# Optimization experiments

Hardware: AMD Instinct MI355X
Metric: run time of the kernel (lower is better)

The kernel has to match this reference:

```python
import jax, jax.numpy as jnp
import numpy as np

SWIGLU_LIMIT = 7.0
ALPHA = 1.702

def swiglu(x):
    # interleaved gate/linear halves, clamped, as in the torch module
    x_glu = x[..., ::2]
    x_lin = x[..., 1::2]
    x_glu = jnp.minimum(x_glu, SWIGLU_LIMIT)
    x_lin = jnp.clip(x_lin, -SWIGLU_LIMIT, SWIGLU_LIMIT)
    return x_glu * jax.nn.sigmoid(ALPHA * x_glu) * (x_lin + 1.0)

def setup_inputs() -> dict:
    key = jax.random.key(0)
    ks = jax.random.split(key, 6)
    B, K, E, H, I = 1024, 4, 16, 2048, 2048
    t = jax.random.normal(ks[0], (B, H), dtype=jnp.float32)
    expert_indices = jax.random.randint(ks[1], (B, K), 0, E, dtype=jnp.int32)
    gate_up_proj = jax.random.normal(ks[2], (E, 2 * I, H), dtype=jnp.float32) * 0.02
    gate_up_proj_bias = jax.random.normal(ks[3], (E, 2 * I), dtype=jnp.float32) * 0.02
    down_proj = jax.random.normal(ks[4], (E, H, I), dtype=jnp.float32) * 0.02
    down_proj_bias = jax.random.normal(ks[5], (E, H), dtype=jnp.float32) * 0.02
    return {"t": t, "expert_indices": expert_indices,
            "gate_up_proj": gate_up_proj, "gate_up_proj_bias": gate_up_proj_bias,
            "down_proj": down_proj, "down_proj_bias": down_proj_bias}

def reference(t, expert_indices, gate_up_proj, gate_up_proj_bias, down_proj, down_proj_bias):
    # Math-equivalent to the torch per-token weight gather: compute every token
    # against every expert, then gather the top_k selected expert outputs.
    # This avoids materializing the [B, K, 2I, H] gathered weight tensor.
    h = jnp.einsum('eck,bk->bec', gate_up_proj, t) + gate_up_proj_bias[None]  # [B,E,2I]
    h = swiglu(h)                                                              # [B,E,I]
    o = jnp.einsum('eck,bek->bec', down_proj, h) + down_proj_bias[None]        # [B,E,H]
    out = jnp.take_along_axis(o, expert_indices[:, :, None].astype(jnp.int32), axis=1)  # [B,K,H]
    return out
```

## Files before the change

### kernel.cpp

```cpp
#include <hip/hip_runtime.h>

typedef unsigned int uint32;
typedef __attribute__((ext_vector_type(8))) short short8;
typedef __attribute__((ext_vector_type(4))) float floatx4;

#define B_TOK 1024
#define TOPK 4
#define NEXP 16
#define H_DIM 2048
#define I_DIM 2048
#define NSLOT 4096
#define CAP 512
#define C1 4096
#define SLOT_ROWS 8192

#define TM 128
#define TN 128
#define BK 32
#define NTH 256

__device__ __forceinline__ unsigned short f2bf(float x) {
  unsigned int u = __float_as_uint(x);
  u += 0x7fffu + ((u >> 16) & 1u);
  return (unsigned short)(u >> 16);
}

__device__ __forceinline__ uint32 pk2bf(float a, float b) {
  uint32 ua = __float_as_uint(a) + 0x8000u;
  uint32 ub = __float_as_uint(b) + 0x8000u;
  return __builtin_amdgcn_perm(ub, ua, 0x07060302u);
}

__global__ void k_setup(const float* __restrict__ t, unsigned short* __restrict__ t_bf,
                        int* __restrict__ sorted_slots, int* __restrict__ counts) {
  int gid = blockIdx.x * blockDim.x + threadIdx.x;
  const float4* tp = (const float4*)t;
  float4 v = tp[gid];
  ushort4 o;
  o.x = f2bf(v.x); o.y = f2bf(v.y); o.z = f2bf(v.z); o.w = f2bf(v.w);
  ((ushort4*)t_bf)[gid] = o;
  if (gid < SLOT_ROWS) sorted_slots[gid] = 0;
  if (gid < NEXP) counts[gid] = 0;
}

__global__ void k_scatter(const int* __restrict__ eidx,
                          int* __restrict__ sorted_slots, int* __restrict__ counts) {
  int slot = blockIdx.x * blockDim.x + threadIdx.x;
  if (slot >= NSLOT) return;
  int e = eidx[slot];
  int j = atomicAdd(counts + e, 1);
  if (j < CAP) sorted_slots[e * CAP + j] = slot;
}

__global__ __launch_bounds__(NTH) void k_gemm1(
    const unsigned short* __restrict__ t_bf, const float* __restrict__ Wg,
    const float* __restrict__ bg, const int* __restrict__ sorted_slots,
    const int* __restrict__ counts, unsigned short* __restrict__ h_act) {
  const int e = blockIdx.y >> 2;
  const int m0 = (blockIdx.y & 3) * TM;
  int cnt = counts[e]; cnt = cnt > CAP ? CAP : cnt;
  if (m0 >= cnt) return;
  const int mr = min(cnt - m0, TM);
  const int c0 = blockIdx.x * TN;
  const int base = e * CAP + m0;

  __shared__ unsigned short smA[2][TM * BK];
  __shared__ unsigned short smB[2][TN * BK];

  const int tid = threadIdx.x;
  const int kq = tid & 3;
  const int r0 = tid >> 2;
  const int r1 = r0 + 64;
  const int sw = (r0 >> 1) & 3;

  const int tok0 = sorted_slots[base + r0] >> 2;
  const int tok1 = sorted_slots[base + r1] >> 2;
  const unsigned short* pA0 = t_bf + (size_t)tok0 * H_DIM + kq * 8;
  const unsigned short* pA1 = t_bf + (size_t)tok1 * H_DIM + kq * 8;
  const float* pB0 = Wg + ((size_t)e * C1 + (size_t)(c0 + r0)) * H_DIM + kq * 8;
  const float* pB1 = Wg + ((size_t)e * C1 + (size_t)(c0 + r1)) * H_DIM + kq * 8;

  const int offA0 = r0 * BK + (kq ^ sw) * 8;
  const int offA1 = r1 * BK + (kq ^ sw) * 8;
  const int offB0 = offA0;
  const int offB1 = offA1;

  const int wave = tid >> 6;
  const int lane = tid & 63;
  const int wm = wave & 1, wn = wave >> 1;
  const int l15 = lane & 15;
  const int kc = lane >> 4;
  const int kcs = (kc ^ ((l15 >> 1) & 3)) * 8;

  floatx4 acc[4][4];
#pragma unroll
  for (int i = 0; i < 4; ++i)
#pragma unroll
    for (int j = 0; j < 4; ++j) acc[i][j] = (floatx4){0.f, 0.f, 0.f, 0.f};

  uint4 a0 = *(const uint4*)(pA0);
  uint4 a1 = *(const uint4*)(pA1);
  float4 b00 = *(const float4*)(pB0);
  float4 b01 = *(const float4*)(pB0 + 4);
  float4 b10 = *(const float4*)(pB1);
  float4 b11 = *(const float4*)(pB1 + 4);
  {
    *(uint4*)&smA[0][offA0] = a0;
    *(uint4*)&smA[0][offA1] = a1;
    uint4 w0, w1;
    w0.x = pk2bf(b00.x, b00.y); w0.y = pk2bf(b00.z, b00.w);
    w0.z = pk2bf(b01.x, b01.y); w0.w = pk2bf(b01.z, b01.w);
    w1.x = pk2bf(b10.x, b10.y); w1.y = pk2bf(b10.z, b10.w);
    w1.z = pk2bf(b11.x, b11.y); w1.w = pk2bf(b11.z, b11.w);
    *(uint4*)&smB[0][offB0] = w0;
    *(uint4*)&smB[0][offB1] = w1;
  }

  const int nk = H_DIM / BK;
#pragma unroll 2
  for (int kk = 0; kk < nk; ++kk) {
    __syncthreads();
    const int buf = kk & 1;
    const bool more = (kk + 1) < nk;
    if (more) {
      const int ko = (kk + 1) * BK;
      a0 = *(const uint4*)(pA0 + ko);
      a1 = *(const uint4*)(pA1 + ko);
      b00 = *(const float4*)(pB0 + ko);
      b01 = *(const float4*)(pB0 + ko + 4);
      b10 = *(const float4*)(pB1 + ko);
      b11 = *(const float4*)(pB1 + ko + 4);
    }
    short8 af[4], bfr[4];
#pragma unroll
    for (int i = 0; i < 4; ++i)
      af[i] = *(const short8*)&smA[buf][(wm * 64 + i * 16 + l15) * BK + kcs];
#pragma unroll
    for (int j = 0; j < 4; ++j)
      bfr[j] = *(const short8*)&smB[buf][(wn * 64 + j * 16 + l15) * BK + kcs];
#pragma unroll
    for (int i = 0; i < 4; ++i)
#pragma unroll
      for (int j = 0; j < 4; ++j)
        acc[i][j] = __builtin_amdgcn_mfma_f32_16x16x32_bf16(af[i], bfr[j], acc[i][j], 0, 0, 0);
    if (more) {
      *(uint4*)&smA[buf ^ 1][offA0] = a0;
      *(uint4*)&smA[buf ^ 1][offA1] = a1;
      uint4 w0, w1;
      w0.x = pk2bf(b00.x, b00.y); w0.y = pk2bf(b00.z, b00.w);
      w0.z = pk2bf(b01.x, b01.y); w0.w = pk2bf(b01.z, b01.w);
      w1.x = pk2bf(b10.x, b10.y); w1.y = pk2bf(b10.z, b10.w);
      w1.z = pk2bf(b11.x, b11.y); w1.w = pk2bf(b11.z, b11.w);
      *(uint4*)&smB[buf ^ 1][offB0] = w0;
      *(uint4*)&smB[buf ^ 1][offB1] = w1;
    }
  }

  const int rq = (lane >> 4) * 4;
#pragma unroll
  for (int j = 0; j < 4; ++j) {
    const int c = c0 + wn * 64 + j * 16 + l15;
    const float bias = bg[e * C1 + c];
    const int ic = c >> 1;
#pragma unroll
    for (int i = 0; i < 4; ++i) {
      const int rbase = wm * 64 + i * 16 + rq;
#pragma unroll
      for (int r = 0; r < 4; ++r) {
        float v = acc[i][j][r] + bias;
        float o = __shfl_xor(v, 1);
        if ((lane & 1) == 0) {
          float xg = fminf(v, 7.0f);
          float xl = fminf(fmaxf(o, -7.0f), 7.0f);
          float res = (xg / (1.0f + __expf(-1.702f * xg))) * (xl + 1.0f);
          const int rl = rbase + r;
          if (rl < mr) h_act[(size_t)(base + rl) * I_DIM + ic] = f2bf(res);
        }
      }
    }
  }
}

__global__ __launch_bounds__(NTH) void k_gemm2(
    const unsigned short* __restrict__ h_act, const float* __restrict__ Wd,
    const float* __restrict__ bd, const int* __restrict__ sorted_slots,
    const int* __restrict__ counts, float* __restrict__ out) {
  const int e = blockIdx.y >> 2;
  const int m0 = (blockIdx.y & 3) * TM;
  int cnt = counts[e]; cnt = cnt > CAP ? CAP : cnt;
  if (m0 >= cnt) return;
  const int mr = min(cnt - m0, TM);
  const int c0 = blockIdx.x * TN;
  const int base = e * CAP + m0;

  __shared__ unsigned short smA[2][TM * BK];
  __shared__ unsigned short smB[2][TN * BK];

  const int tid = threadIdx.x;
  const int kq = tid & 3;
  const int r0 = tid >> 2;
  const int r1 = r0 + 64;
  const int sw = (r0 >> 1) & 3;

  const unsigned short* pA0 = h_act + (size_t)(base + r0) * I_DIM + kq * 8;
  const unsigned short* pA1 = h_act + (size_t)(base + r1) * I_DIM + kq * 8;
  const float* pB0 = Wd + ((size_t)e * H_DIM + (size_t)(c0 + r0)) * I_DIM + kq * 8;
  const float* pB1 = Wd + ((size_t)e * H_DIM + (size_t)(c0 + r1)) * I_DIM + kq * 8;

  const int offA0 = r0 * BK + (kq ^ sw) * 8;
  const int offA1 = r1 * BK + (kq ^ sw) * 8;

  const int wave = tid >> 6;
  const int lane = tid & 63;
  const int wm = wave & 1, wn = wave >> 1;
  const int l15 = lane & 15;
  const int kc = lane >> 4;
  const int kcs = (kc ^ ((l15 >> 1) & 3)) * 8;

  floatx4 acc[4][4];
#pragma unroll
  for (int i = 0; i < 4; ++i)
#pragma unroll
    for (int j = 0; j < 4; ++j) acc[i][j] = (floatx4){0.f, 0.f, 0.f, 0.f};

  uint4 a0 = *(const uint4*)(pA0);
  uint4 a1 = *(const uint4*)(pA1);
  float4 b00 = *(const float4*)(pB0);
  float4 b01 = *(const float4*)(pB0 + 4);
  float4 b10 = *(const float4*)(pB1);
  float4 b11 = *(const float4*)(pB1 + 4);
  {
    *(uint4*)&smA[0][offA0] = a0;
    *(uint4*)&smA[0][offA1] = a1;
    uint4 w0, w1;
    w0.x = pk2bf(b00.x, b00.y); w0.y = pk2bf(b00.z, b00.w);
    w0.z = pk2bf(b01.x, b01.y); w0.w = pk2bf(b01.z, b01.w);
    w1.x = pk2bf(b10.x, b10.y); w1.y = pk2bf(b10.z, b10.w);
    w1.z = pk2bf(b11.x, b11.y); w1.w = pk2bf(b11.z, b11.w);
    *(uint4*)&smB[0][offA0] = w0;
    *(uint4*)&smB[0][offA1] = w1;
  }

  const int nk = I_DIM / BK;
#pragma unroll 2
  for (int kk = 0; kk < nk; ++kk) {
    __syncthreads();
    const int buf = kk & 1;
    const bool more = (kk + 1) < nk;
    if (more) {
      const int ko = (kk + 1) * BK;
      a0 = *(const uint4*)(pA0 + ko);
      a1 = *(const uint4*)(pA1 + ko);
      b00 = *(const float4*)(pB0 + ko);
      b01 = *(const float4*)(pB0 + ko + 4);
      b10 = *(const float4*)(pB1 + ko);
      b11 = *(const float4*)(pB1 + ko + 4);
    }
    short8 af[4], bfr[4];
#pragma unroll
    for (int i = 0; i < 4; ++i)
      af[i] = *(const short8*)&smA[buf][(wm * 64 + i * 16 + l15) * BK + kcs];
#pragma unroll
    for (int j = 0; j < 4; ++j)
      bfr[j] = *(const short8*)&smB[buf][(wn * 64 + j * 16 + l15) * BK + kcs];
#pragma unroll
    for (int i = 0; i < 4; ++i)
#pragma unroll
      for (int j = 0; j < 4; ++j)
        acc[i][j] = __builtin_amdgcn_mfma_f32_16x16x32_bf16(af[i], bfr[j], acc[i][j], 0, 0, 0);
    if (more) {
      *(uint4*)&smA[buf ^ 1][offA0] = a0;
      *(uint4*)&smA[buf ^ 1][offA1] = a1;
      uint4 w0, w1;
      w0.x = pk2bf(b00.x, b00.y); w0.y = pk2bf(b00.z, b00.w);
      w0.z = pk2bf(b01.x, b01.y); w0.w = pk2bf(b01.z, b01.w);
      w1.x = pk2bf(b10.x, b10.y); w1.y = pk2bf(b10.z, b10.w);
      w1.z = pk2bf(b11.x, b11.y); w1.w = pk2bf(b11.z, b11.w);
      *(uint4*)&smB[buf ^ 1][offA0] = w0;
      *(uint4*)&smB[buf ^ 1][offA1] = w1;
    }
  }

  const int rq = (lane >> 4) * 4;
#pragma unroll
  for (int j = 0; j < 4; ++j) {
    const int c = c0 + wn * 64 + j * 16 + l15;
    const float bias = bd[e * H_DIM + c];
#pragma unroll
    for (int i = 0; i < 4; ++i) {
      const int rbase = wm * 64 + i * 16 + rq;
#pragma unroll
      for (int r = 0; r < 4; ++r) {
        const int rl = rbase + r;
        if (rl < mr) {
          const int slot = sorted_slots[base + rl];
          out[(size_t)slot * H_DIM + c] = acc[i][j][r] + bias;
        }
      }
    }
  }
}

extern "C" void kernel_launch(void* const* d_in, const int* in_sizes, int n_in,
                              void* d_out, int out_size, void* d_ws, size_t ws_size,
                              hipStream_t stream) {
  const float* t = (const float*)d_in[0];
  const int* eidx = (const int*)d_in[1];
  const float* Wg = (const float*)d_in[2];
  const float* bg = (const float*)d_in[3];
  const float* Wd = (const float*)d_in[4];
  const float* bd = (const float*)d_in[5];
  float* out = (float*)d_out;

  char* ws = (char*)d_ws;
  unsigned short* t_bf = (unsigned short*)ws;
  unsigned short* h_act = (unsigned short*)(ws + (size_t)4 * 1024 * 1024);
  int* sorted_slots = (int*)(ws + (size_t)36 * 1024 * 1024);
  int* counts = (int*)(ws + (size_t)36 * 1024 * 1024 + (size_t)SLOT_ROWS * 4);

  k_setup<<<dim3((B_TOK * H_DIM / 4) / 256), dim3(256), 0, stream>>>(t, t_bf, sorted_slots, counts);
  k_scatter<<<dim3(NSLOT / 256), dim3(256), 0, stream>>>(eidx, sorted_slots, counts);
  k_gemm1<<<dim3(C1 / TN, NEXP * (CAP / TM)), dim3(NTH), 0, stream>>>(t_bf, Wg, bg, sorted_slots, counts, h_act);
  k_gemm2<<<dim3(H_DIM / TN, NEXP * (CAP / TM)), dim3(NTH), 0, stream>>>(h_act, Wd, bd, sorted_slots, counts, out);
}
```

Before: 1.068 ms.

## Pre-convert expert weights to bf16 and stage tiles with direct global-to-LDS loads

Both weight tensors are converted from fp32 to bf16 once per call. Wg is converted inside the setup kernel, and Wd is converted by extra blocks prepended to the first GEMM grid. The GEMM main loops then stream bf16 tiles straight into LDS with global_load_lds, using pre-swizzled source addresses. This removes the per-tile fp32 loads, register staging and pack conversions, which should lower register pressure and VALU work in the inner loop. The cost is an extra full-weight read/write pass plus large workspace buffers, and the grid now mixes conversion blocks with GEMM blocks.

```diff
diff --git a/kernel.cpp b/kernel.cpp
--- a/kernel.cpp
+++ b/kernel.cpp
@@ -18,6 +18,9 @@
 #define TN 128
 #define BK 32
 #define NTH 256
+#define CVT_Y 16
+#define N8_WG (NEXP * C1 * H_DIM / 8)
+#define N8_WD (NEXP * H_DIM * I_DIM / 8)
 
 __device__ __forceinline__ unsigned short f2bf(float x) {
   unsigned int u = __float_as_uint(x);
@@ -31,8 +34,16 @@
   return __builtin_amdgcn_perm(ub, ua, 0x07060302u);
 }
 
-__global__ void k_setup(const float* __restrict__ t, unsigned short* __restrict__ t_bf,
-                        int* __restrict__ sorted_slots, int* __restrict__ counts) {
+typedef const unsigned int __attribute__((address_space(1))) cu32_g;
+typedef unsigned int __attribute__((address_space(3))) u32_l;
+__device__ __forceinline__ void ldst16(void* lds, const void* g) {
+  __builtin_amdgcn_global_load_lds((cu32_g*)g, (u32_l*)lds, 16, 0, 0);
+}
+
+__global__ __launch_bounds__(256) void k_setup(
+    const float* __restrict__ t, unsigned short* __restrict__ t_bf,
+    int* __restrict__ sorted_slots, int* __restrict__ counts,
+    const float* __restrict__ Wg, unsigned short* __restrict__ Wg_bf) {
   int gid = blockIdx.x * blockDim.x + threadIdx.x;
   const float4* tp = (const float4*)t;
   float4 v = tp[gid];
@@ -41,6 +52,17 @@
   ((ushort4*)t_bf)[gid] = o;
   if (gid < SLOT_ROWS) sorted_slots[gid] = 0;
   if (gid < NEXP) counts[gid] = 0;
+
+  const float4* s4 = (const float4*)Wg;
+  uint4* d4 = (uint4*)Wg_bf;
+  const int stride = gridDim.x * 256;
+  for (int i = gid; i < N8_WG; i += stride) {
+    float4 v0 = s4[2 * i], v1 = s4[2 * i + 1];
+    uint4 w;
+    w.x = pk2bf(v0.x, v0.y); w.y = pk2bf(v0.z, v0.w);
+    w.z = pk2bf(v1.x, v1.y); w.w = pk2bf(v1.z, v1.w);
+    d4[i] = w;
+  }
 }
 
 __global__ void k_scatter(const int* __restrict__ eidx,
@@ -52,12 +74,34 @@
   if (j < CAP) sorted_slots[e * CAP + j] = slot;
 }
 
+#define STAGE1(bb, ko)                                              \
+  ldst16(&smA[bb][(wave * 16) * BK], pA0 + (ko));                   \
+  ldst16(&smA[bb][(64 + wave * 16) * BK], pA1 + (ko));              \
+  ldst16(&smB[bb][(wave * 16) * BK], pB0 + (ko));                   \
+  ldst16(&smB[bb][(64 + wave * 16) * BK], pB1 + (ko));
+
 __global__ __launch_bounds__(NTH) void k_gemm1(
-    const unsigned short* __restrict__ t_bf, const float* __restrict__ Wg,
+    const unsigned short* __restrict__ t_bf, const unsigned short* __restrict__ Wg_bf,
     const float* __restrict__ bg, const int* __restrict__ sorted_slots,
-    const int* __restrict__ counts, unsigned short* __restrict__ h_act) {
-  const int e = blockIdx.y >> 2;
-  const int m0 = (blockIdx.y & 3) * TM;
+    const int* __restrict__ counts, unsigned short* __restrict__ h_act,
+    const float* __restrict__ Wd, unsigned short* __restrict__ Wd_bf) {
+  if (blockIdx.y < CVT_Y) {
+    int i = (blockIdx.y * gridDim.x + blockIdx.x) * NTH + threadIdx.x;
+    const int stride = CVT_Y * (C1 / TN) * NTH;
+    const float4* s4 = (const float4*)Wd;
+    uint4* d4 = (uint4*)Wd_bf;
+    for (; i < N8_WD; i += stride) {
+      float4 v0 = s4[2 * i], v1 = s4[2 * i + 1];
+      uint4 w;
+      w.x = pk2bf(v0.x, v0.y); w.y = pk2bf(v0.z, v0.w);
+      w.z = pk2bf(v1.x, v1.y); w.w = pk2bf(v1.z, v1.w);
+      d4[i] = w;
+    }
+    return;
+  }
+  const int yb = blockIdx.y - CVT_Y;
+  const int e = yb >> 2;
+  const int m0 = (yb & 3) * TM;
   int cnt = counts[e]; cnt = cnt > CAP ? CAP : cnt;
   if (m0 >= cnt) return;
   const int mr = min(cnt - m0, TM);
@@ -72,18 +116,7 @@
   const int r0 = tid >> 2;
   const int r1 = r0 + 64;
   const int sw = (r0 >> 1) & 3;
-
-  const int tok0 = sorted_slots[base + r0] >> 2;
-  const int tok1 = sorted_slots[base + r1] >> 2;
-  const unsigned short* pA0 = t_bf + (size_t)tok0 * H_DIM + kq * 8;
-  const unsigned short* pA1 = t_bf + (size_t)tok1 * H_DIM + kq * 8;
-  const float* pB0 = Wg + ((size_t)e * C1 + (size_t)(c0 + r0)) * H_DIM + kq * 8;
-  const float* pB1 = Wg + ((size_t)e * C1 + (size_t)(c0 + r1)) * H_DIM + kq * 8;
-
-  const int offA0 = r0 * BK + (kq ^ sw) * 8;
-  const int offA1 = r1 * BK + (kq ^ sw) * 8;
-  const int offB0 = offA0;
-  const int offB1 = offA1;
+  const int q8 = (kq ^ sw) * 8;
 
   const int wave = tid >> 6;
   const int lane = tid & 63;
@@ -92,44 +125,28 @@
   const int kc = lane >> 4;
   const int kcs = (kc ^ ((l15 >> 1) & 3)) * 8;
 
+  const int tok0 = sorted_slots[base + r0] >> 2;
+  const int tok1 = sorted_slots[base + r1] >> 2;
+  const unsigned short* pA0 = t_bf + (size_t)tok0 * H_DIM + q8;
+  const unsigned short* pA1 = t_bf + (size_t)tok1 * H_DIM + q8;
+  const unsigned short* pB0 = Wg_bf + ((size_t)e * C1 + (size_t)(c0 + r0)) * H_DIM + q8;
+  const unsigned short* pB1 = Wg_bf + ((size_t)e * C1 + (size_t)(c0 + r1)) * H_DIM + q8;
+
   floatx4 acc[4][4];
 #pragma unroll
   for (int i = 0; i < 4; ++i)
 #pragma unroll
     for (int j = 0; j < 4; ++j) acc[i][j] = (floatx4){0.f, 0.f, 0.f, 0.f};
 
-  uint4 a0 = *(const uint4*)(pA0);
-  uint4 a1 = *(const uint4*)(pA1);
-  float4 b00 = *(const float4*)(pB0);
-  float4 b01 = *(const float4*)(pB0 + 4);
-  float4 b10 = *(const float4*)(pB1);
-  float4 b11 = *(const float4*)(pB1 + 4);
-  {
-    *(uint4*)&smA[0][offA0] = a0;
-    *(uint4*)&smA[0][offA1] = a1;
-    uint4 w0, w1;
-    w0.x = pk2bf(b00.x, b00.y); w0.y = pk2bf(b00.z, b00.w);
-    w0.z = pk2bf(b01.x, b01.y); w0.w = pk2bf(b01.z, b01.w);
-    w1.x = pk2bf(b10.x, b10.y); w1.y = pk2bf(b10.z, b10.w);
-    w1.z = pk2bf(b11.x, b11.y); w1.w = pk2bf(b11.z, b11.w);
-    *(uint4*)&smB[0][offB0] = w0;
-    *(uint4*)&smB[0][offB1] = w1;
-  }
-
+  STAGE1(0, 0);
   const int nk = H_DIM / BK;
 #pragma unroll 2
   for (int kk = 0; kk < nk; ++kk) {
     __syncthreads();
     const int buf = kk & 1;
-    const bool more = (kk + 1) < nk;
-    if (more) {
+    if (kk + 1 < nk) {
       const int ko = (kk + 1) * BK;
-      a0 = *(const uint4*)(pA0 + ko);
-      a1 = *(const uint4*)(pA1 + ko);
-      b00 = *(const float4*)(pB0 + ko);
-      b01 = *(const float4*)(pB0 + ko + 4);
-      b10 = *(const float4*)(pB1 + ko);
-      b11 = *(const float4*)(pB1 + ko + 4);
+      if (buf == 0) { STAGE1(1, ko); } else { STAGE1(0, ko); }
     }
     short8 af[4], bfr[4];
 #pragma unroll
@@ -143,17 +160,6 @@
 #pragma unroll
       for (int j = 0; j < 4; ++j)
         acc[i][j] = __builtin_amdgcn_mfma_f32_16x16x32_bf16(af[i], bfr[j], acc[i][j], 0, 0, 0);
-    if (more) {
-      *(uint4*)&smA[buf ^ 1][offA0] = a0;
-      *(uint4*)&smA[buf ^ 1][offA1] = a1;
-      uint4 w0, w1;
-      w0.x = pk2bf(b00.x, b00.y); w0.y = pk2bf(b00.z, b00.w);
-      w0.z = pk2bf(b01.x, b01.y); w0.w = pk2bf(b01.z, b01.w);
-      w1.x = pk2bf(b10.x, b10.y); w1.y = pk2bf(b10.z, b10.w);
-      w1.z = pk2bf(b11.x, b11.y); w1.w = pk2bf(b11.z, b11.w);
-      *(uint4*)&smB[buf ^ 1][offB0] = w0;
-      *(uint4*)&smB[buf ^ 1][offB1] = w1;
-    }
   }
 
   const int rq = (lane >> 4) * 4;
@@ -182,7 +188,7 @@
 }
 
 __global__ __launch_bounds__(NTH) void k_gemm2(
-    const unsigned short* __restrict__ h_act, const float* __restrict__ Wd,
+    const unsigned short* __restrict__ h_act, const unsigned short* __restrict__ Wd_bf,
     const float* __restrict__ bd, const int* __restrict__ sorted_slots,
     const int* __restrict__ counts, float* __restrict__ out) {
   const int e = blockIdx.y >> 2;
@@ -201,14 +207,7 @@
   const int r0 = tid >> 2;
   const int r1 = r0 + 64;
   const int sw = (r0 >> 1) & 3;
-
-  const unsigned short* pA0 = h_act + (size_t)(base + r0) * I_DIM + kq * 8;
-  const unsigned short* pA1 = h_act + (size_t)(base + r1) * I_DIM + kq * 8;
-  const float* pB0 = Wd + ((size_t)e * H_DIM + (size_t)(c0 + r0)) * I_DIM + kq * 8;
-  const float* pB1 = Wd + ((size_t)e * H_DIM + (size_t)(c0 + r1)) * I_DIM + kq * 8;
-
-  const int offA0 = r0 * BK + (kq ^ sw) * 8;
-  const int offA1 = r1 * BK + (kq ^ sw) * 8;
+  const int q8 = (kq ^ sw) * 8;
 
   const int wave = tid >> 6;
   const int lane = tid & 63;
@@ -217,44 +216,26 @@
   const int kc = lane >> 4;
   const int kcs = (kc ^ ((l15 >> 1) & 3)) * 8;
 
+  const unsigned short* pA0 = h_act + (size_t)(base + r0) * I_DIM + q8;
+  const unsigned short* pA1 = h_act + (size_t)(base + r1) * I_DIM + q8;
+  const unsigned short* pB0 = Wd_bf + ((size_t)e * H_DIM + (size_t)(c0 + r0)) * I_DIM + q8;
+  const unsigned short* pB1 = Wd_bf + ((size_t)e * H_DIM + (size_t)(c0 + r1)) * I_DIM + q8;
+
   floatx4 acc[4][4];
 #pragma unroll
   for (int i = 0; i < 4; ++i)
 #pragma unroll
     for (int j = 0; j < 4; ++j) acc[i][j] = (floatx4){0.f, 0.f, 0.f, 0.f};
 
-  uint4 a0 = *(const uint4*)(pA0);
-  uint4 a1 = *(const uint4*)(pA1);
-  float4 b00 = *(const float4*)(pB0);
-  float4 b01 = *(const float4*)(pB0 + 4);
-  float4 b10 = *(const float4*)(pB1);
-  float4 b11 = *(const float4*)(pB1 + 4);
-  {
-    *(uint4*)&smA[0][offA0] = a0;
-    *(uint4*)&smA[0][offA1] = a1;
-    uint4 w0, w1;
-    w0.x = pk2bf(b00.x, b00.y); w0.y = pk2bf(b00.z, b00.w);
-    w0.z = pk2bf(b01.x, b01.y); w0.w = pk2bf(b01.z, b01.w);
-    w1.x = pk2bf(b10.x, b10.y); w1.y = pk2bf(b10.z, b10.w);
-    w1.z = pk2bf(b11.x, b11.y); w1.w = pk2bf(b11.z, b11.w);
-    *(uint4*)&smB[0][offA0] = w0;
-    *(uint4*)&smB[0][offA1] = w1;
-  }
-
+  STAGE1(0, 0);
   const int nk = I_DIM / BK;
 #pragma unroll 2
   for (int kk = 0; kk < nk; ++kk) {
     __syncthreads();
     const int buf = kk & 1;
-    const bool more = (kk + 1) < nk;
-    if (more) {
+    if (kk + 1 < nk) {
       const int ko = (kk + 1) * BK;
-      a0 = *(const uint4*)(pA0 + ko);
-      a1 = *(const uint4*)(pA1 + ko);
-      b00 = *(const float4*)(pB0 + ko);
-      b01 = *(const float4*)(pB0 + ko + 4);
-      b10 = *(const float4*)(pB1 + ko);
-      b11 = *(const float4*)(pB1 + ko + 4);
+      if (buf == 0) { STAGE1(1, ko); } else { STAGE1(0, ko); }
     }
     short8 af[4], bfr[4];
 #pragma unroll
@@ -268,17 +249,6 @@
 #pragma unroll
       for (int j = 0; j < 4; ++j)
         acc[i][j] = __builtin_amdgcn_mfma_f32_16x16x32_bf16(af[i], bfr[j], acc[i][j], 0, 0, 0);
-    if (more) {
-      *(uint4*)&smA[buf ^ 1][offA0] = a0;
-      *(uint4*)&smA[buf ^ 1][offA1] = a1;
-      uint4 w0, w1;
-      w0.x = pk2bf(b00.x, b00.y); w0.y = pk2bf(b00.z, b00.w);
-      w0.z = pk2bf(b01.x, b01.y); w0.w = pk2bf(b01.z, b01.w);
-      w1.x = pk2bf(b10.x, b10.y); w1.y = pk2bf(b10.z, b10.w);
-      w1.z = pk2bf(b11.x, b11.y); w1.w = pk2bf(b11.z, b11.w);
-      *(uint4*)&smB[buf ^ 1][offA0] = w0;
-      *(uint4*)&smB[buf ^ 1][offA1] = w1;
-    }
   }
 
   const int rq = (lane >> 4) * 4;
@@ -317,9 +287,11 @@
   unsigned short* h_act = (unsigned short*)(ws + (size_t)4 * 1024 * 1024);
   int* sorted_slots = (int*)(ws + (size_t)36 * 1024 * 1024);
   int* counts = (int*)(ws + (size_t)36 * 1024 * 1024 + (size_t)SLOT_ROWS * 4);
-
-  k_setup<<<dim3((B_TOK * H_DIM / 4) / 256), dim3(256), 0, stream>>>(t, t_bf, sorted_slots, counts);
+  unsigned short* Wg_bf = (unsigned short*)(ws + (size_t)48 * 1024 * 1024);
+  unsigned short* Wd_bf = (unsigned short*)(ws + (size_t)304 * 1024 * 1024);
+
+  k_setup<<<dim3((B_TOK * H_DIM / 4) / 256), dim3(256), 0, stream>>>(t, t_bf, sorted_slots, counts, Wg, Wg_bf);
   k_scatter<<<dim3(NSLOT / 256), dim3(256), 0, stream>>>(eidx, sorted_slots, counts);
-  k_gemm1<<<dim3(C1 / TN, NEXP * (CAP / TM)), dim3(NTH), 0, stream>>>(t_bf, Wg, bg, sorted_slots, counts, h_act);
-  k_gemm2<<<dim3(H_DIM / TN, NEXP * (CAP / TM)), dim3(NTH), 0, stream>>>(h_act, Wd, bd, sorted_slots, counts, out);
-}
+  k_gemm1<<<dim3(C1 / TN, CVT_Y + NEXP * (CAP / TM)), dim3(NTH), 0, stream>>>(t_bf, Wg_bf, bg, sorted_slots, counts, h_act, Wd, Wd_bf);
+  k_gemm2<<<dim3(H_DIM / TN, NEXP * (CAP / TM)), dim3(NTH), 0, stream>>>(h_act, Wd_bf, bd, sorted_slots, counts, out);
+}
```

Result: slower. 1.222 ms (+14.5%).
